# Optimization experiments

Hardware: AMD Instinct MI355X
Metric: run time of the kernel (lower is better)

The kernel has to match this reference:

```python
import jax, jax.numpy as jnp
import numpy as np

N = 80000
E = 1280000
C_IN, HID, C_OUT = 3, 64, 1
DEPTH = 3
KS = [40000, 20000, 10000]  # ceil(0.5 * n) per pooling level
EPS = 1e-5


def gcn_conv(x, W, src, dst, ew, n, fill=2.0):
    # PyG GCNConv with add_self_loops=True; improved => self-loop weight fill=2.0
    h = x @ W                                           # [n, F]
    deg = jax.ops.segment_sum(ew, dst, num_segments=n) + fill
    dinv = jax.lax.rsqrt(deg)
    norm = dinv[src] * ew * dinv[dst]                   # [E]
    agg = jax.ops.segment_sum(norm[:, None] * h[src], dst, num_segments=n)
    return agg + (fill * dinv * dinv)[:, None] * h      # self-loop term


def batchnorm(x, gamma, beta):
    # BatchNorm1d in training mode: biased batch stats over the node dim
    mu = jnp.mean(x, axis=0)
    var = jnp.var(x, axis=0)
    return gamma * (x - mu) * jax.lax.rsqrt(var + EPS) + beta


def gcn_block(x, src, dst, ew, n, W, gamma, beta, fill=2.0):
    return jax.nn.relu(batchnorm(gcn_conv(x, W, src, dst, ew, n, fill), gamma, beta))


def topk_pool(x, src, dst, ew, w, k):
    # TopKPooling with ReLU nonlinearity: score = relu(x.w / ||w||)
    n = x.shape[0]
    score = jax.nn.relu(x @ w / jnp.linalg.norm(w))
    sc, perm = jax.lax.top_k(score, k)
    xk = x[perm] * sc[:, None]
    # filter_adj with fixed edge count: invalid edges get weight 0 (no-op in GCN)
    mapping = jnp.full((n,), -1, dtype=src.dtype).at[perm].set(
        jnp.arange(k, dtype=src.dtype))
    ns, nd = mapping[src], mapping[dst]
    valid = (ns >= 0) & (nd >= 0)
    ns = jnp.where(valid, ns, 0)
    nd = jnp.where(valid, nd, 0)
    new_ew = jnp.where(valid, ew, jnp.zeros((), ew.dtype))
    return xk, ns, nd, new_ew, perm


def _forward(x, edge_index, Wd, gd, bd, pw, Wu, gu, bu, W_out):
    src, dst = edge_index[0], edge_index[1]
    ew = jnp.ones(src.shape, x.dtype)
    n = x.shape[0]
    x = gcn_block(x, src, dst, ew, n, Wd[0], gd[0], bd[0])
    xs, sds, ews, perms = [x], [(src, dst)], [ew], []
    for i in range(DEPTH):
        x, src, dst, ew, perm = topk_pool(x, src, dst, ew, pw[i], KS[i])
        x = gcn_block(x, src, dst, ew, KS[i], Wd[i + 1], gd[i + 1], bd[i + 1])
        if i < DEPTH - 1:
            xs.append(x); sds.append((src, dst)); ews.append(ew)
        perms.append(perm)
    for i in range(DEPTH):
        j = DEPTH - 1 - i
        res = xs[j]; src, dst = sds[j]; ew = ews[j]; perm = perms[j]
        up = jnp.zeros_like(res).at[perm].set(x)
        x = res + up
        if i < DEPTH - 1:
            x = gcn_block(x, src, dst, ew, res.shape[0], Wu[i], gu[i], bu[i])
        else:
            x = jax.nn.sigmoid(
                gcn_conv(x, W_out, src, dst, ew, res.shape[0], fill=1.0))
    return x


def setup_inputs() -> dict:
    key = jax.random.key(0)
    ks = jax.random.split(key, 16)
    nrm = lambda k, shape: jax.random.normal(k, shape, jnp.float32) * 0.1
    inp = {
        "x": jax.random.normal(ks[0], (N, C_IN), jnp.float32),
        "edge_index": jax.random.randint(ks[1], (2, E), 0, N, jnp.int32),
    }
    dims = [(C_IN, HID)] + [(HID, HID)] * DEPTH
    ki = 2
    for l, (a, b) in enumerate(dims):
        inp[f"W_d{l}"] = nrm(ks[ki], (a, b)); ki += 1
        inp[f"g_d{l}"] = jnp.ones((b,), jnp.float32)
        inp[f"b_d{l}"] = jnp.zeros((b,), jnp.float32)
    for l in range(DEPTH):
        inp[f"pw{l}"] = nrm(ks[ki], (HID,)); ki += 1
    for l in range(DEPTH - 1):
        inp[f"W_u{l}"] = nrm(ks[ki], (HID, HID)); ki += 1
        inp[f"g_u{l}"] = jnp.ones((HID,), jnp.float32)
        inp[f"b_u{l}"] = jnp.zeros((HID,), jnp.float32)
    inp["W_out"] = nrm(ks[ki], (HID, C_OUT))
    return inp


def reference(x, edge_index, W_d0, g_d0, b_d0, W_d1, g_d1, b_d1, W_d2, g_d2,
              b_d2, W_d3, g_d3, b_d3, pw0, pw1, pw2, W_u0, g_u0, b_u0,
              W_u1, g_u1, b_u1, W_out):
    Wd = [W_d0, W_d1, W_d2, W_d3]
    gd = [g_d0, g_d1, g_d2, g_d3]
    bd = [b_d0, b_d1, b_d2, b_d3]
    pw = [pw0, pw1, pw2]
    Wu = [W_u0, W_u1]
    gu = [g_u0, g_u1]
    bu = [b_u0, b_u1]
    return _forward(x, edge_index, Wd, gd, bd, pw, Wu, gu, bu, W_out)
```

## Files before the change

### kernel.cpp

```cpp
#include <hip/hip_runtime.h>
#include <cstdint>

#define NN0 80000
#define NE 1280000
#define MMB_GRID 2048
#define EB 2048
#define ENB 625

static inline int cdiv(int a, int b){ return (a+b-1)/b; }

__global__ void k_ehist6(const int* __restrict__ key, int* __restrict__ hist, int shift){
  __shared__ int lh[64];
  if (threadIdx.x < 64) lh[threadIdx.x] = 0;
  __syncthreads();
  int base = blockIdx.x*EB + threadIdx.x;
  #pragma unroll
  for (int u = 0; u < 8; u++)
    atomicAdd(&lh[(key[base + u*256] >> shift) & 63], 1);
  __syncthreads();
  if (threadIdx.x < 64) hist[threadIdx.x*ENB + blockIdx.x] = lh[threadIdx.x];
}

__global__ void k_scan_part(const int* __restrict__ in, int* __restrict__ bsum, int n){
  __shared__ int ws[256];
  int base = blockIdx.x*2048 + threadIdx.x*8;
  int s = 0;
  #pragma unroll
  for (int u = 0; u < 8; u++){ int i = base+u; if (i < n) s += in[i]; }
  ws[threadIdx.x] = s; __syncthreads();
  for (int st = 128; st > 0; st >>= 1){
    if (threadIdx.x < st) ws[threadIdx.x] += ws[threadIdx.x+st];
    __syncthreads();
  }
  if (threadIdx.x == 0) bsum[blockIdx.x] = ws[0];
}

__global__ void k_scan_fin_flat(int* __restrict__ data, const int* __restrict__ bsum, int nb, int n){
  __shared__ int bws[256]; __shared__ int ws[256];
  int t = threadIdx.x;
  bws[t] = (t < nb) ? bsum[t] : 0; __syncthreads();
  for (int st = 1; st < 256; st <<= 1){
    int a = (t >= st) ? bws[t-st] : 0; __syncthreads();
    bws[t] += a; __syncthreads();
  }
  int blockoff = (blockIdx.x == 0) ? 0 : bws[blockIdx.x-1];
  int base = blockIdx.x*2048 + t*8;
  int v[8]; int s = 0;
  #pragma unroll
  for (int u = 0; u < 8; u++){ int i = base+u; v[u] = (i < n) ? data[i] : 0; s += v[u]; }
  ws[t] = s; __syncthreads();
  for (int st = 1; st < 256; st <<= 1){
    int a = (t >= st) ? ws[t-st] : 0; __syncthreads();
    ws[t] += a; __syncthreads();
  }
  int off = blockoff + ws[t] - s;
  #pragma unroll
  for (int u = 0; u < 8; u++){
    int i = base+u;
    if (i < n){ data[i] = off; off += v[u]; }
  }
}

__global__ void k_escatter6(const int* __restrict__ keyin, const int* __restrict__ valin,
                            int* __restrict__ keyout, int* __restrict__ valout,
                            const int* __restrict__ hist, int shift){
  __shared__ int dbase[64], run[64], wcnt[4][64];
  int t = threadIdx.x, lane = t & 63, w = t >> 6;
  if (t < 64){ dbase[t] = hist[t*ENB + blockIdx.x]; run[t] = 0; }
  __syncthreads();
  for (int u = 0; u < 8; u++){
    if (t < 64){ wcnt[0][t]=0; wcnt[1][t]=0; wcnt[2][t]=0; wcnt[3][t]=0; }
    __syncthreads();
    int g = blockIdx.x*EB + u*256 + t;
    int kk = keyin[g], vv = valin[g];
    int d = (kk >> shift) & 63;
    unsigned long long m = ~0ull;
    #pragma unroll
    for (int b = 0; b < 6; b++){
      unsigned long long bal = __ballot((d >> b) & 1);
      m &= ((d >> b) & 1) ? bal : ~bal;
    }
    int rnk = __popcll(m & ((1ull << lane) - 1ull));
    if (rnk == 0) wcnt[w][d] = __popcll(m);
    __syncthreads();
    int off2 = run[d] + rnk;
    for (int w2 = 0; w2 < w; w2++) off2 += wcnt[w2][d];
    int pos = dbase[d] + off2;
    keyout[pos] = kk; valout[pos] = vv;
    __syncthreads();
    if (t < 64) run[t] += wcnt[0][t] + wcnt[1][t] + wcnt[2][t] + wcnt[3][t];
    __syncthreads();
  }
}

__global__ __launch_bounds__(1024) void k_bucket_build(
    const int* __restrict__ ek, const int* __restrict__ ev,
    const int* __restrict__ hist_s,
    int* __restrict__ rp, int* __restrict__ col,
    float* __restrict__ dA, float* __restrict__ dB, int n){
  __shared__ int cnt[2048];
  __shared__ int sa[1024], sb[1024];
  int b = blockIdx.x, t = threadIdx.x;
  int gb = hist_s[b*ENB];
  int ge = hist_s[(b+1)*ENB];
  int n0 = b*2048;
  cnt[t] = 0; cnt[t+1024] = 0;
  __syncthreads();
  for (int e = gb + t; e < ge; e += 1024)
    atomicAdd(&cnt[ek[e] - n0], 1);
  __syncthreads();
  int v0 = cnt[2*t], v1 = cnt[2*t+1];
  int s = v0 + v1;
  sa[t] = s; __syncthreads();
  int* cu = sa; int* ot = sb;
  for (int st = 1; st < 1024; st <<= 1){
    ot[t] = cu[t] + ((t >= st) ? cu[t-st] : 0);
    __syncthreads();
    int* tmp = cu; cu = ot; ot = tmp;
  }
  int base2 = cu[t] - s;
  int p0 = base2, p1 = base2 + v0;
  int nn = n - n0; if (nn > 2048) nn = 2048;
  cnt[2*t]   = gb + p0;
  cnt[2*t+1] = gb + p1;
  int i0 = n0 + 2*t;
  if (2*t < nn){
    rp[i0] = gb + p0;
    dA[i0] = 1.0f/sqrtf((float)v0 + 2.f);
    dB[i0] = 1.0f/sqrtf((float)v0 + 1.f);
  }
  if (2*t+1 < nn){
    rp[i0+1] = gb + p1;
    dA[i0+1] = 1.0f/sqrtf((float)v1 + 2.f);
    dB[i0+1] = 1.0f/sqrtf((float)v1 + 1.f);
  }
  if (b == (int)gridDim.x - 1 && t == 0) rp[n] = ge;
  __syncthreads();
  for (int e = gb + t; e < ge; e += 1024){
    int d = ek[e];
    int pos = atomicAdd(&cnt[d - n0], 1);
    col[pos] = ev[e];
  }
}

__global__ void k_scan_rp(const int* __restrict__ in, int* __restrict__ rp,
                          int* __restrict__ cur, float* __restrict__ dA,
                          float* __restrict__ dB, int n){
  __shared__ int ws[256];
  int t = threadIdx.x;
  int pre = blockIdx.x*2048;
  int s = 0;
  for (int i = t; i < pre; i += 256) s += in[i];
  ws[t] = s; __syncthreads();
  for (int st = 128; st > 0; st >>= 1){
    if (t < st) ws[t] += ws[t+st];
    __syncthreads();
  }
  int blockoff = ws[0];
  __syncthreads();
  int base = pre + t*8;
  int v[8]; int ls = 0;
  #pragma unroll
  for (int u = 0; u < 8; u++){ int i = base+u; v[u] = (i < n) ? in[i] : 0; ls += v[u]; }
  ws[t] = ls; __syncthreads();
  for (int st = 1; st < 256; st <<= 1){
    int a = (t >= st) ? ws[t-st] : 0; __syncthreads();
    ws[t] += a; __syncthreads();
  }
  int off = blockoff + ws[t] - ls;
  #pragma unroll
  for (int u = 0; u < 8; u++){
    int i = base+u;
    if (i < n){
      rp[i] = off;
      if (cur) cur[i] = off;
      off += v[u];
      dA[i] = 1.0f/sqrtf((float)v[u] + 2.f);
      if (dB) dB[i] = 1.0f/sqrtf((float)v[u] + 1.f);
      if (i == n-1) rp[n] = off;
    }
  }
}

__global__ void k_conv64(const int* __restrict__ rp, const int* __restrict__ col,
                         const float* __restrict__ dinv, const float* __restrict__ x,
                         const float* __restrict__ W, float* __restrict__ out,
                         float* __restrict__ part, int n){
  __shared__ float yl[4][64];
  __shared__ float ls[64], lq[64];
  int lane = threadIdx.x & 63, w = threadIdx.x >> 6;
  if (threadIdx.x < 64){ ls[threadIdx.x] = 0.f; lq[threadIdx.x] = 0.f; }
  __syncthreads();
  float sa = 0.f, sq = 0.f;
  int wid = blockIdx.x*4 + w, nw = gridDim.x*4;
  for (int i = wid; i < n; i += nw){
    int beg = rp[i], end = rp[i+1];
    float di = dinv[i];
    float y = 0.f;
    int j = beg;
    for (; j + 4 <= end; j += 4){
      int s0 = col[j], s1 = col[j+1], s2 = col[j+2], s3 = col[j+3];
      float y0 = dinv[s0]*x[s0*64+lane];
      float y1 = dinv[s1]*x[s1*64+lane];
      float y2 = dinv[s2]*x[s2*64+lane];
      float y3 = dinv[s3]*x[s3*64+lane];
      y += (y0+y1) + (y2+y3);
    }
    for (; j < end; j++){ int s = col[j]; y += dinv[s]*x[s*64+lane]; }
    y = di*y + 2.f*di*di*x[i*64+lane];
    yl[w][lane] = y;
    float acc = 0.f;
    #pragma unroll
    for (int k2 = 0; k2 < 64; k2++)
      acc += yl[w][k2]*W[k2*64+lane];
    out[i*64+lane] = acc;
    sa += acc; sq += acc*acc;
  }
  atomicAdd(&ls[lane], sa); atomicAdd(&lq[lane], sq);
  __syncthreads();
  if (threadIdx.x < 128)
    part[blockIdx.x*128 + threadIdx.x] =
      (threadIdx.x < 64) ? ls[threadIdx.x] : lq[threadIdx.x-64];
}

__global__ void k_conv3(const int* __restrict__ rp, const int* __restrict__ col,
                        const float* __restrict__ dinv, const float* __restrict__ x,
                        const float* __restrict__ W, float* __restrict__ out,
                        float* __restrict__ part, int n){
  __shared__ float ls[64], lq[64];
  int lane = threadIdx.x & 63, w = threadIdx.x >> 6;
  if (threadIdx.x < 64){ ls[threadIdx.x] = 0.f; lq[threadIdx.x] = 0.f; }
  __syncthreads();
  float wf0 = W[lane], wf1 = W[64+lane], wf2 = W[128+lane];
  float sa = 0.f, sq = 0.f;
  int wid = blockIdx.x*4 + w, nw = gridDim.x*4;
  for (int i = wid; i < n; i += nw){
    int beg = rp[i], end = rp[i+1];
    float a0 = 0.f, a1 = 0.f, a2 = 0.f;
    for (int j = beg + lane; j < end; j += 64){
      int s2 = col[j];
      float ds = dinv[s2];
      a0 += ds*x[s2*3+0]; a1 += ds*x[s2*3+1]; a2 += ds*x[s2*3+2];
    }
    for (int o = 32; o > 0; o >>= 1){
      a0 += __shfl_xor(a0, o); a1 += __shfl_xor(a1, o); a2 += __shfl_xor(a2, o);
    }
    float di = dinv[i];
    float sl = 2.f*di*di;
    a0 = di*a0 + sl*x[i*3+0];
    a1 = di*a1 + sl*x[i*3+1];
    a2 = di*a2 + sl*x[i*3+2];
    float s = a0*wf0 + a1*wf1 + a2*wf2;
    out[i*64+lane] = s; sa += s; sq += s*s;
  }
  atomicAdd(&ls[lane], sa); atomicAdd(&lq[lane], sq);
  __syncthreads();
  if (threadIdx.x < 128)
    part[blockIdx.x*128 + threadIdx.x] =
      (threadIdx.x < 64) ? ls[threadIdx.x] : lq[threadIdx.x-64];
}

__global__ void k_stats_reduce(const float* __restrict__ part, float* __restrict__ stats){
  int c = blockIdx.x, lane = threadIdx.x;
  float s = 0.f;
  for (int b = lane; b < MMB_GRID; b += 64) s += part[b*128 + c];
  for (int o = 32; o > 0; o >>= 1) s += __shfl_xor(s, o);
  if (lane == 0) stats[c] = s;
}

__global__ void k_bnrelu_score(float* __restrict__ x, const float* __restrict__ stats,
                               const float* __restrict__ gamma, const float* __restrict__ beta,
                               const float* __restrict__ pw,
                               float* __restrict__ score, unsigned* __restrict__ key,
                               int* __restrict__ idx, int n, int P){
  int lane = threadIdx.x & 63, w = threadIdx.x >> 6;
  int wid = blockIdx.x*4 + w, nw = gridDim.x*4;
  float inv_n = 1.f/(float)n;
  float mu = stats[lane]*inv_n;
  float var = stats[64+lane]*inv_n - mu*mu;
  float gs = gamma[lane]*(1.f/sqrtf(var+1e-5f));
  float bt = beta[lane];
  float pv = pw[lane];
  float q = pv*pv;
  for (int o = 32; o > 0; o >>= 1) q += __shfl_xor(q, o);
  float qn = 1.f/sqrtf(q);
  for (int i = wid; i < n; i += nw){
    float v = fmaxf(gs*(x[i*64+lane]-mu)+bt, 0.f);
    x[i*64+lane] = v;
    float s = v*pv;
    for (int o = 32; o > 0; o >>= 1) s += __shfl_xor(s, o);
    if (lane == 0){
      float sc = fmaxf(s*qn, 0.f);
      score[i] = sc; key[i] = ~__float_as_uint(sc); idx[i] = i;
    }
  }
  for (int g = n + wid; g < P; g += nw)
    if (lane == 0){ key[g] = 0xFFFFFFFFu; idx[g] = 0; }
}

__global__ void k_radix_hist(const unsigned* __restrict__ key, int* __restrict__ hist,
                             int shift, int nblk){
  __shared__ int lh[256];
  lh[threadIdx.x] = 0; __syncthreads();
  int base = blockIdx.x*1024 + threadIdx.x;
  #pragma unroll
  for (int u = 0; u < 4; u++){
    unsigned d = (key[base + u*256] >> shift) & 255u;
    atomicAdd(&lh[d], 1);
  }
  __syncthreads();
  hist[threadIdx.x*nblk + blockIdx.x] = lh[threadIdx.x];
}

__global__ void k_radix_scatter(const unsigned* __restrict__ keyin, const int* __restrict__ idxin,
                                unsigned* __restrict__ keyout, int* __restrict__ idxout,
                                const int* __restrict__ hist, int shift, int nblk){
  __shared__ int dbase[256], run[256], sc[256];
  __shared__ int wcnt[4][256];
  int t = threadIdx.x, lane = t & 63, w = t >> 6;
  int pre = 0, tot = 0;
  for (int b = 0; b < nblk; b++){
    int v = hist[t*nblk + b];
    if (b < blockIdx.x) pre += v;
    tot += v;
  }
  sc[t] = tot; __syncthreads();
  for (int st = 1; st < 256; st <<= 1){
    int a = (t >= st) ? sc[t-st] : 0; __syncthreads();
    sc[t] += a; __syncthreads();
  }
  dbase[t] = sc[t] - tot + pre;
  run[t] = 0;
  for (int u = 0; u < 4; u++){
    wcnt[0][t] = 0; wcnt[1][t] = 0; wcnt[2][t] = 0; wcnt[3][t] = 0;
    __syncthreads();
    int g = blockIdx.x*1024 + u*256 + t;
    unsigned kk = keyin[g]; int id = idxin[g];
    unsigned d = (kk >> shift) & 255u;
    unsigned long long m = ~0ull;
    #pragma unroll
    for (int b = 0; b < 8; b++){
      unsigned long long bal = __ballot((d >> b) & 1u);
      m &= ((d >> b) & 1u) ? bal : ~bal;
    }
    int rnk = __popcll(m & ((1ull << lane) - 1ull));
    if (rnk == 0) wcnt[w][d] = __popcll(m);
    __syncthreads();
    int off2 = run[d] + rnk;
    for (int w2 = 0; w2 < w; w2++) off2 += wcnt[w2][d];
    int pos = dbase[d] + off2;
    keyout[pos] = kk; idxout[pos] = id;
    __syncthreads();
    run[t] += wcnt[0][t] + wcnt[1][t] + wcnt[2][t] + wcnt[3][t];
    __syncthreads();
  }
}

__global__ void k_select_gather(const int* __restrict__ idxs, const float* __restrict__ x,
                                const float* __restrict__ score, int* __restrict__ perm,
                                int* __restrict__ mapv, float* __restrict__ xk, int n, int k){
  int t = blockIdx.x*blockDim.x + threadIdx.x;
  if (t < n){
    int i = idxs[t];
    mapv[i] = (t < k) ? t : -1;
    if (t < k) perm[t] = i;
  }
  if (t < k*64){
    int r = t >> 6, f = t & 63;
    int i = idxs[r];
    xk[t] = x[i*64+f]*score[i];
  }
}

__global__ void k_hist_mapped(const int* __restrict__ rp_p, const int* __restrict__ col_p,
                              const int* __restrict__ mapv, int* __restrict__ indeg, int np){
  int d = blockIdx.x*blockDim.x + threadIdx.x;
  if (d >= np) return;
  int md = mapv[d];
  if (md < 0) return;
  int c = 0, e = rp_p[d+1];
  int j = rp_p[d];
  for (; j + 4 <= e; j += 4){
    int c0 = (mapv[col_p[j]]   >= 0);
    int c1 = (mapv[col_p[j+1]] >= 0);
    int c2 = (mapv[col_p[j+2]] >= 0);
    int c3 = (mapv[col_p[j+3]] >= 0);
    c += (c0+c1) + (c2+c3);
  }
  for (; j < e; j++) if (mapv[col_p[j]] >= 0) c++;
  indeg[md] = c;
}

__global__ void k_scatter_mapped(const int* __restrict__ rp_p, const int* __restrict__ col_p,
                                 const int* __restrict__ mapv, const int* __restrict__ rp_c,
                                 int* __restrict__ col_c, int np){
  int d = blockIdx.x*blockDim.x + threadIdx.x;
  if (d >= np) return;
  int md = mapv[d];
  if (md < 0) return;
  int pos = rp_c[md], e = rp_p[d+1];
  int j = rp_p[d];
  for (; j + 4 <= e; j += 4){
    int m0 = mapv[col_p[j]], m1 = mapv[col_p[j+1]];
    int m2 = mapv[col_p[j+2]], m3 = mapv[col_p[j+3]];
    if (m0 >= 0) col_c[pos++] = m0;
    if (m1 >= 0) col_c[pos++] = m1;
    if (m2 >= 0) col_c[pos++] = m2;
    if (m3 >= 0) col_c[pos++] = m3;
  }
  for (; j < e; j++){
    int ms = mapv[col_p[j]];
    if (ms >= 0) col_c[pos++] = ms;
  }
}

__global__ void k_bnrelu_scatter(const float* __restrict__ x, const float* __restrict__ stats,
                                 const float* __restrict__ gamma, const float* __restrict__ beta,
                                 const int* __restrict__ perm, float* __restrict__ res, int n){
  int t = blockIdx.x*blockDim.x + threadIdx.x;
  if (t >= n*64) return;
  int r = t >> 6, f = t & 63;
  float inv_n = 1.0f/(float)n;
  float mu = stats[f]*inv_n;
  float var = stats[64+f]*inv_n - mu*mu;
  float v = gamma[f]*(x[t]-mu)*(1.0f/sqrtf(var+1e-5f)) + beta[f];
  res[perm[r]*64+f] += fmaxf(v, 0.f);
}

__global__ void k_matvec(const float* __restrict__ x, const float* __restrict__ W,
                         float* __restrict__ h1, int n){
  int lane = threadIdx.x & 63, w = threadIdx.x >> 6;
  int wid = blockIdx.x*4 + w, nw = gridDim.x*4;
  float wv = W[lane];
  for (int i = wid; i < n; i += nw){
    float v = x[i*64+lane]*wv;
    for (int o = 32; o > 0; o >>= 1) v += __shfl_xor(v, o);
    if (lane == 0) h1[i] = v;
  }
}

__global__ void k_gather_sig(const int* __restrict__ rp, const int* __restrict__ col,
                             const float* __restrict__ dinv, const float* __restrict__ h1,
                             float* __restrict__ out, int n){
  int i = blockIdx.x*blockDim.x + threadIdx.x;
  if (i >= n) return;
  int beg = rp[i], end = rp[i+1];
  float di = dinv[i];
  float acc = 0.f;
  int j = beg;
  for (; j + 4 <= end; j += 4){
    int s0 = col[j], s1 = col[j+1], s2 = col[j+2], s3 = col[j+3];
    float v0 = dinv[s0]*h1[s0];
    float v1 = dinv[s1]*h1[s1];
    float v2 = dinv[s2]*h1[s2];
    float v3 = dinv[s3]*h1[s3];
    acc += (v0+v1) + (v2+v3);
  }
  for (; j < end; j++) acc += dinv[col[j]]*h1[col[j]];
  float v = di*acc + di*di*h1[i];
  out[i] = 1.f/(1.f+expf(-v));
}


extern "C" void kernel_launch(void* const* d_in, const int* in_sizes, int n_in,
                              void* d_out, int out_size, void* d_ws, size_t ws_size,
                              hipStream_t stream) {
  const float* x_in = (const float*)d_in[0];
  const int* ei = (const int*)d_in[1];
  const int* src0 = ei;
  const int* dst0 = ei + NE;
  const float* W_d[4] = {(const float*)d_in[2],(const float*)d_in[5],(const float*)d_in[8],(const float*)d_in[11]};
  const float* g_d[4] = {(const float*)d_in[3],(const float*)d_in[6],(const float*)d_in[9],(const float*)d_in[12]};
  const float* b_d[4] = {(const float*)d_in[4],(const float*)d_in[7],(const float*)d_in[10],(const float*)d_in[13]};
  const float* pw[3]  = {(const float*)d_in[14],(const float*)d_in[15],(const float*)d_in[16]};
  const float* W_u[2] = {(const float*)d_in[17],(const float*)d_in[20]};
  const float* g_u[2] = {(const float*)d_in[18],(const float*)d_in[21]};
  const float* b_u[2] = {(const float*)d_in[19],(const float*)d_in[22]};
  const float* W_out  = (const float*)d_in[23];
  float* out = (float*)d_out;

  float* base = (float*)d_ws;
  size_t off = 0;
  auto alloc = [&](size_t nf){ float* p = base + off; off += nf; return p; };
  float* x0 = alloc(5120000);
  float* x1 = alloc(2560000);
  float* x2 = alloc(1280000);
  float* x3 = alloc(640000);
  float* A  = alloc(2560000);
  int* col0 = (int*)alloc(NE);
  int* col1 = (int*)alloc(NE);
  int* col2 = (int*)alloc(NE);
  int* col3 = (int*)alloc(NE);
  int* ek1 = (int*)alloc(NE);
  int* ev1 = (int*)alloc(NE);
  int* rp0 = (int*)alloc(80001);
  int* rp1 = (int*)alloc(40001);
  int* rp2 = (int*)alloc(20001);
  int* rp3 = (int*)alloc(10001);
  int* indeg  = (int*)alloc(NN0);
  float* dinv0  = alloc(NN0);
  float* dinv0f = alloc(NN0);
  float* dinv1  = alloc(40000);
  float* dinv2  = alloc(20000);
  float* dinv3  = alloc(10000);
  float* score = alloc(NN0);
  int* mapv = (int*)alloc(NN0);
  int* p0 = (int*)alloc(40000);
  int* p1 = (int*)alloc(20000);
  int* p2 = (int*)alloc(10000);
  float* stats = alloc(128);
  float* part  = alloc(MMB_GRID*128);
  unsigned* keyA = (unsigned*)alloc(81920);
  unsigned* keyB = (unsigned*)alloc(81920);
  int* idxA = (int*)alloc(81920);
  int* idxB = (int*)alloc(81920);
  int* hist = (int*)alloc(81920);
  int* ehist = (int*)alloc(64*ENB);
  int* bsum = (int*)alloc(256);
  (void)ws_size; (void)in_sizes; (void)n_in; (void)out_size;

  const int B = 256;

  k_ehist6<<<ENB, B, 0, stream>>>(dst0, ehist, 11);
  {
    int nb = cdiv(64*ENB, 2048);
    k_scan_part    <<<nb, B, 0, stream>>>(ehist, bsum, 64*ENB);
    k_scan_fin_flat<<<nb, B, 0, stream>>>(ehist, bsum, nb, 64*ENB);
  }
  k_escatter6<<<ENB, B, 0, stream>>>(dst0, src0, ek1, ev1, ehist, 11);
  k_bucket_build<<<cdiv(NN0,2048), 1024, 0, stream>>>(ek1, ev1, ehist, rp0, col0,
                                                      dinv0, dinv0f, NN0);

  auto conv = [&](const float* xin, const float* W, int n,
                  const int* rp, const int* col, const float* dv, float* dstb){
    k_conv64<<<MMB_GRID, B, 0, stream>>>(rp, col, dv, xin, W, dstb, part, n);
    k_stats_reduce<<<128, 64, 0, stream>>>(part, stats);
  };

  auto pool = [&](float* xb, const float* gm, const float* bt, const float* pwv,
                  int n, int k, int* pm){
    int nblk = cdiv(n, 1024), P = nblk*1024;
    k_bnrelu_score<<<1024, B, 0, stream>>>(xb, stats, gm, bt, pwv, score, keyA, idxA, n, P);
    unsigned* ka = keyA; int* ia = idxA; unsigned* kb = keyB; int* ib = idxB;
    for (int pass = 0; pass < 4; pass++){
      k_radix_hist   <<<nblk, B, 0, stream>>>(ka, hist, pass*8, nblk);
      k_radix_scatter<<<nblk, B, 0, stream>>>(ka, ia, kb, ib, hist, pass*8, nblk);
      unsigned* tk = ka; ka = kb; kb = tk;
      int* ti = ia; ia = ib; ib = ti;
    }
    k_select_gather<<<cdiv(k*64,B), B, 0, stream>>>(ia, xb, score, pm, mapv, A, n, k);
  };

  auto csr_mapped = [&](const int* rp_p, const int* col_p, int np, int nc,
                        int* rp_c, int* col_c, float* dv){
    k_hist_mapped<<<cdiv(np,B), B, 0, stream>>>(rp_p, col_p, mapv, indeg, np);
    k_scan_rp<<<cdiv(nc,2048), B, 0, stream>>>(indeg, rp_c, nullptr, dv, nullptr, nc);
    k_scatter_mapped<<<cdiv(np,B), B, 0, stream>>>(rp_p, col_p, mapv, rp_c, col_c, np);
  };

  k_conv3<<<MMB_GRID, B, 0, stream>>>(rp0, col0, dinv0, x_in, W_d[0], x0, part, NN0);
  k_stats_reduce<<<128, 64, 0, stream>>>(part, stats);
  pool(x0, g_d[0], b_d[0], pw[0], NN0, 40000, p0);
  csr_mapped(rp0, col0, NN0, 40000, rp1, col1, dinv1);

  conv(A, W_d[1], 40000, rp1, col1, dinv1, x1);
  pool(x1, g_d[1], b_d[1], pw[1], 40000, 20000, p1);
  csr_mapped(rp1, col1, 40000, 20000, rp2, col2, dinv2);

  conv(A, W_d[2], 20000, rp2, col2, dinv2, x2);
  pool(x2, g_d[2], b_d[2], pw[2], 20000, 10000, p2);
  csr_mapped(rp2, col2, 20000, 10000, rp3, col3, dinv3);

  conv(A, W_d[3], 10000, rp3, col3, dinv3, x3);

  k_bnrelu_scatter<<<cdiv(10000*64,B), B, 0, stream>>>(x3, stats, g_d[3], b_d[3], p2, x2, 10000);
  conv(x2, W_u[0], 20000, rp2, col2, dinv2, A);
  k_bnrelu_scatter<<<cdiv(20000*64,B), B, 0, stream>>>(A, stats, g_u[0], b_u[0], p1, x1, 20000);
  conv(x1, W_u[1], 40000, rp1, col1, dinv1, A);
  k_bnrelu_scatter<<<cdiv(40000*64,B), B, 0, stream>>>(A, stats, g_u[1], b_u[1], p0, x0, 40000);

  float* h1 = score;
  k_matvec<<<512, B, 0, stream>>>(x0, W_out, h1, NN0);
  k_gather_sig<<<cdiv(NN0,B), B, 0, stream>>>(rp0, col0, dinv0f, h1, out, NN0);
}
```

Baseline: 743.2 us.

## Use 11-bit radix top-k with fused histogram/gather and global-atomic CSR build

Replaces the 4-pass 8-bit radix sort for top-k with three 11-bit passes. The first histogram is fused into the BN/ReLU/score kernel, and the final scatter directly writes perm, mapping and the scaled gathered features, dropping the separate select/gather kernel. The level-0 CSR build now counts in-degrees with global atomics during the edge bucketing, then scans and scatters with global atomic cursors instead of the shared-memory bucket builder. Conv grid sizes also now scale with the graph level. The changes cut kernel launches and passes, but add larger shared histograms, 11-iteration ballot ranking, and global atomic contention on the edge scatter.

```diff
diff --git a/kernel.cpp b/kernel.cpp
--- a/kernel.cpp
+++ b/kernel.cpp
@@ -3,13 +3,17 @@
 
 #define NN0 80000
 #define NE 1280000
-#define MMB_GRID 2048
 #define EB 2048
 #define ENB 625
+#define RD 2048
+#define RDM 2047
 
 static inline int cdiv(int a, int b){ return (a+b-1)/b; }
 
-__global__ void k_ehist6(const int* __restrict__ key, int* __restrict__ hist, int shift){
+__global__ void k_ehist6(const int* __restrict__ key, int* __restrict__ hist, int shift,
+                         int* __restrict__ indeg){
+  for (int i = blockIdx.x*blockDim.x + threadIdx.x; i < NN0; i += gridDim.x*blockDim.x)
+    indeg[i] = 0;
   __shared__ int lh[64];
   if (threadIdx.x < 64) lh[threadIdx.x] = 0;
   __syncthreads();
@@ -63,7 +67,8 @@
 
 __global__ void k_escatter6(const int* __restrict__ keyin, const int* __restrict__ valin,
                             int* __restrict__ keyout, int* __restrict__ valout,
-                            const int* __restrict__ hist, int shift){
+                            const int* __restrict__ hist, int shift,
+                            int* __restrict__ indeg){
   __shared__ int dbase[64], run[64], wcnt[4][64];
   int t = threadIdx.x, lane = t & 63, w = t >> 6;
   if (t < 64){ dbase[t] = hist[t*ENB + blockIdx.x]; run[t] = 0; }
@@ -87,58 +92,18 @@
     for (int w2 = 0; w2 < w; w2++) off2 += wcnt[w2][d];
     int pos = dbase[d] + off2;
     keyout[pos] = kk; valout[pos] = vv;
+    atomicAdd(&indeg[kk], 1);
     __syncthreads();
     if (t < 64) run[t] += wcnt[0][t] + wcnt[1][t] + wcnt[2][t] + wcnt[3][t];
     __syncthreads();
   }
 }
 
-__global__ __launch_bounds__(1024) void k_bucket_build(
-    const int* __restrict__ ek, const int* __restrict__ ev,
-    const int* __restrict__ hist_s,
-    int* __restrict__ rp, int* __restrict__ col,
-    float* __restrict__ dA, float* __restrict__ dB, int n){
-  __shared__ int cnt[2048];
-  __shared__ int sa[1024], sb[1024];
-  int b = blockIdx.x, t = threadIdx.x;
-  int gb = hist_s[b*ENB];
-  int ge = hist_s[(b+1)*ENB];
-  int n0 = b*2048;
-  cnt[t] = 0; cnt[t+1024] = 0;
-  __syncthreads();
-  for (int e = gb + t; e < ge; e += 1024)
-    atomicAdd(&cnt[ek[e] - n0], 1);
-  __syncthreads();
-  int v0 = cnt[2*t], v1 = cnt[2*t+1];
-  int s = v0 + v1;
-  sa[t] = s; __syncthreads();
-  int* cu = sa; int* ot = sb;
-  for (int st = 1; st < 1024; st <<= 1){
-    ot[t] = cu[t] + ((t >= st) ? cu[t-st] : 0);
-    __syncthreads();
-    int* tmp = cu; cu = ot; ot = tmp;
-  }
-  int base2 = cu[t] - s;
-  int p0 = base2, p1 = base2 + v0;
-  int nn = n - n0; if (nn > 2048) nn = 2048;
-  cnt[2*t]   = gb + p0;
-  cnt[2*t+1] = gb + p1;
-  int i0 = n0 + 2*t;
-  if (2*t < nn){
-    rp[i0] = gb + p0;
-    dA[i0] = 1.0f/sqrtf((float)v0 + 2.f);
-    dB[i0] = 1.0f/sqrtf((float)v0 + 1.f);
-  }
-  if (2*t+1 < nn){
-    rp[i0+1] = gb + p1;
-    dA[i0+1] = 1.0f/sqrtf((float)v1 + 2.f);
-    dB[i0+1] = 1.0f/sqrtf((float)v1 + 1.f);
-  }
-  if (b == (int)gridDim.x - 1 && t == 0) rp[n] = ge;
-  __syncthreads();
-  for (int e = gb + t; e < ge; e += 1024){
+__global__ void k_escat_local(const int* __restrict__ ek, const int* __restrict__ ev,
+                              int* __restrict__ cur, int* __restrict__ col){
+  for (int e = blockIdx.x*blockDim.x + threadIdx.x; e < NE; e += gridDim.x*blockDim.x){
     int d = ek[e];
-    int pos = atomicAdd(&cnt[d - n0], 1);
+    int pos = atomicAdd(&cur[d], 1);
     col[pos] = ev[e];
   }
 }
@@ -260,10 +225,10 @@
       (threadIdx.x < 64) ? ls[threadIdx.x] : lq[threadIdx.x-64];
 }
 
-__global__ void k_stats_reduce(const float* __restrict__ part, float* __restrict__ stats){
+__global__ void k_stats_reduce(const float* __restrict__ part, float* __restrict__ stats, int nb){
   int c = blockIdx.x, lane = threadIdx.x;
   float s = 0.f;
-  for (int b = lane; b < MMB_GRID; b += 64) s += part[b*128 + c];
+  for (int b = lane; b < nb; b += 64) s += part[b*128 + c];
   for (int o = 32; o > 0; o >>= 1) s += __shfl_xor(s, o);
   if (lane == 0) stats[c] = s;
 }
@@ -272,9 +237,12 @@
                                const float* __restrict__ gamma, const float* __restrict__ beta,
                                const float* __restrict__ pw,
                                float* __restrict__ score, unsigned* __restrict__ key,
-                               int* __restrict__ idx, int n, int P){
-  int lane = threadIdx.x & 63, w = threadIdx.x >> 6;
-  int wid = blockIdx.x*4 + w, nw = gridDim.x*4;
+                               int* __restrict__ idx, int* __restrict__ hist,
+                               int n, int nblk){
+  __shared__ int lh[RD];
+  int t = threadIdx.x, lane = t & 63, w = t >> 6;
+  #pragma unroll
+  for (int j = 0; j < 8; j++) lh[t*8+j] = 0;
   float inv_n = 1.f/(float)n;
   float mu = stats[lane]*inv_n;
   float var = stats[64+lane]*inv_n - mu*mu;
@@ -284,64 +252,106 @@
   float q = pv*pv;
   for (int o = 32; o > 0; o >>= 1) q += __shfl_xor(q, o);
   float qn = 1.f/sqrtf(q);
-  for (int i = wid; i < n; i += nw){
-    float v = fmaxf(gs*(x[i*64+lane]-mu)+bt, 0.f);
-    x[i*64+lane] = v;
-    float s = v*pv;
-    for (int o = 32; o > 0; o >>= 1) s += __shfl_xor(s, o);
-    if (lane == 0){
-      float sc = fmaxf(s*qn, 0.f);
-      score[i] = sc; key[i] = ~__float_as_uint(sc); idx[i] = i;
-    }
-  }
-  for (int g = n + wid; g < P; g += nw)
-    if (lane == 0){ key[g] = 0xFFFFFFFFu; idx[g] = 0; }
-}
-
-__global__ void k_radix_hist(const unsigned* __restrict__ key, int* __restrict__ hist,
-                             int shift, int nblk){
-  __shared__ int lh[256];
-  lh[threadIdx.x] = 0; __syncthreads();
-  int base = blockIdx.x*1024 + threadIdx.x;
-  #pragma unroll
+  __syncthreads();
+  int P = nblk*1024;
+  int base = blockIdx.x*1024 + w*256;
+  for (int t2 = 0; t2 < 256; t2++){
+    int i = base + t2;
+    if (i < n){
+      float v = fmaxf(gs*(x[i*64+lane]-mu)+bt, 0.f);
+      x[i*64+lane] = v;
+      float s = v*pv;
+      for (int o = 32; o > 0; o >>= 1) s += __shfl_xor(s, o);
+      if (lane == 0){
+        float sc = fmaxf(s*qn, 0.f);
+        unsigned kk = ~__float_as_uint(sc);
+        score[i] = sc; key[i] = kk; idx[i] = i;
+        atomicAdd(&lh[kk & RDM], 1);
+      }
+    } else if (i < P){
+      if (lane == 0){
+        key[i] = 0xFFFFFFFFu; idx[i] = 0;
+        atomicAdd(&lh[RDM], 1);
+      }
+    }
+  }
+  __syncthreads();
+  #pragma unroll
+  for (int j = 0; j < 8; j++)
+    hist[(t*8+j)*nblk + blockIdx.x] = lh[t*8+j];
+}
+
+__global__ void k_radix_hist11(const unsigned* __restrict__ key, int* __restrict__ hist,
+                               int shift, int nblk){
+  __shared__ int lh[RD];
+  int t = threadIdx.x;
+  #pragma unroll
+  for (int j = 0; j < 8; j++) lh[t*8+j] = 0;
+  __syncthreads();
+  int base = blockIdx.x*1024 + t;
+  #pragma unroll
+  for (int u = 0; u < 4; u++)
+    atomicAdd(&lh[(key[base + u*256] >> shift) & RDM], 1);
+  __syncthreads();
+  #pragma unroll
+  for (int j = 0; j < 8; j++)
+    hist[(t*8+j)*nblk + blockIdx.x] = lh[t*8+j];
+}
+
+__global__ void k_radix_scatter11(const unsigned* __restrict__ keyin, const int* __restrict__ idxin,
+                                  unsigned* __restrict__ keyout, int* __restrict__ idxout,
+                                  const int* __restrict__ hist, int shift, int nblk,
+                                  int fin, const float* __restrict__ x,
+                                  const float* __restrict__ score,
+                                  int* __restrict__ perm, int* __restrict__ mapv,
+                                  float* __restrict__ xk, int n, int k){
+  __shared__ int dbase[RD], run[RD], wcnt[4][RD];
+  __shared__ int ssum[256], stmp[256];
+  int t = threadIdx.x, lane = t & 63, w = t >> 6;
+  int b = blockIdx.x;
+  int pre[8], tot[8];
+  #pragma unroll
+  for (int j = 0; j < 8; j++){ pre[j] = 0; tot[j] = 0; }
+  for (int blk = 0; blk < nblk; blk++){
+    #pragma unroll
+    for (int j = 0; j < 8; j++){
+      int v = hist[(t*8+j)*nblk + blk];
+      tot[j] += v;
+      if (blk < b) pre[j] += v;
+    }
+  }
+  int S = 0; int ex[8];
+  #pragma unroll
+  for (int j = 0; j < 8; j++){ ex[j] = S; S += tot[j]; }
+  ssum[t] = S; __syncthreads();
+  int* cu = ssum; int* ot = stmp;
+  for (int st = 1; st < 256; st <<= 1){
+    ot[t] = cu[t] + ((t >= st) ? cu[t-st] : 0);
+    __syncthreads();
+    int* tmp = cu; cu = ot; ot = tmp;
+  }
+  int exS = cu[t] - S;
+  #pragma unroll
+  for (int j = 0; j < 8; j++){
+    dbase[t*8+j] = exS + ex[j] + pre[j];
+    run[t*8+j] = 0;
+  }
+  __syncthreads();
   for (int u = 0; u < 4; u++){
-    unsigned d = (key[base + u*256] >> shift) & 255u;
-    atomicAdd(&lh[d], 1);
-  }
-  __syncthreads();
-  hist[threadIdx.x*nblk + blockIdx.x] = lh[threadIdx.x];
-}
-
-__global__ void k_radix_scatter(const unsigned* __restrict__ keyin, const int* __restrict__ idxin,
-                                unsigned* __restrict__ keyout, int* __restrict__ idxout,
-                                const int* __restrict__ hist, int shift, int nblk){
-  __shared__ int dbase[256], run[256], sc[256];
-  __shared__ int wcnt[4][256];
-  int t = threadIdx.x, lane = t & 63, w = t >> 6;
-  int pre = 0, tot = 0;
-  for (int b = 0; b < nblk; b++){
-    int v = hist[t*nblk + b];
-    if (b < blockIdx.x) pre += v;
-    tot += v;
-  }
-  sc[t] = tot; __syncthreads();
-  for (int st = 1; st < 256; st <<= 1){
-    int a = (t >= st) ? sc[t-st] : 0; __syncthreads();
-    sc[t] += a; __syncthreads();
-  }
-  dbase[t] = sc[t] - tot + pre;
-  run[t] = 0;
-  for (int u = 0; u < 4; u++){
-    wcnt[0][t] = 0; wcnt[1][t] = 0; wcnt[2][t] = 0; wcnt[3][t] = 0;
-    __syncthreads();
-    int g = blockIdx.x*1024 + u*256 + t;
+    #pragma unroll
+    for (int j = 0; j < 8; j++){
+      int bb = t*8+j;
+      wcnt[0][bb] = 0; wcnt[1][bb] = 0; wcnt[2][bb] = 0; wcnt[3][bb] = 0;
+    }
+    __syncthreads();
+    int g = b*1024 + u*256 + t;
     unsigned kk = keyin[g]; int id = idxin[g];
-    unsigned d = (kk >> shift) & 255u;
+    int d = (kk >> shift) & RDM;
     unsigned long long m = ~0ull;
     #pragma unroll
-    for (int b = 0; b < 8; b++){
-      unsigned long long bal = __ballot((d >> b) & 1u);
-      m &= ((d >> b) & 1u) ? bal : ~bal;
+    for (int bit = 0; bit < 11; bit++){
+      unsigned long long bal = __ballot((d >> bit) & 1);
+      m &= ((d >> bit) & 1) ? bal : ~bal;
     }
     int rnk = __popcll(m & ((1ull << lane) - 1ull));
     if (rnk == 0) wcnt[w][d] = __popcll(m);
@@ -349,26 +359,30 @@
     int off2 = run[d] + rnk;
     for (int w2 = 0; w2 < w; w2++) off2 += wcnt[w2][d];
     int pos = dbase[d] + off2;
-    keyout[pos] = kk; idxout[pos] = id;
-    __syncthreads();
-    run[t] += wcnt[0][t] + wcnt[1][t] + wcnt[2][t] + wcnt[3][t];
-    __syncthreads();
-  }
-}
-
-__global__ void k_select_gather(const int* __restrict__ idxs, const float* __restrict__ x,
-                                const float* __restrict__ score, int* __restrict__ perm,
-                                int* __restrict__ mapv, float* __restrict__ xk, int n, int k){
-  int t = blockIdx.x*blockDim.x + threadIdx.x;
-  if (t < n){
-    int i = idxs[t];
-    mapv[i] = (t < k) ? t : -1;
-    if (t < k) perm[t] = i;
-  }
-  if (t < k*64){
-    int r = t >> 6, f = t & 63;
-    int i = idxs[r];
-    xk[t] = x[i*64+f]*score[i];
+    if (!fin){
+      keyout[pos] = kk; idxout[pos] = id;
+    } else if (pos < n){
+      mapv[id] = (pos < k) ? pos : -1;
+      if (pos < k){
+        perm[pos] = id;
+        float sc = score[id];
+        const float4* xr = (const float4*)(x + (size_t)id*64);
+        float4* xo = (float4*)(xk + (size_t)pos*64);
+        #pragma unroll
+        for (int f = 0; f < 16; f++){
+          float4 vv = xr[f];
+          vv.x *= sc; vv.y *= sc; vv.z *= sc; vv.w *= sc;
+          xo[f] = vv;
+        }
+      }
+    }
+    __syncthreads();
+    #pragma unroll
+    for (int j = 0; j < 8; j++){
+      int bb = t*8+j;
+      run[bb] += wcnt[0][bb] + wcnt[1][bb] + wcnt[2][bb] + wcnt[3][bb];
+    }
+    __syncthreads();
   }
 }
 
@@ -497,6 +511,7 @@
   int* rp1 = (int*)alloc(40001);
   int* rp2 = (int*)alloc(20001);
   int* rp3 = (int*)alloc(10001);
+  int* cur0 = (int*)alloc(NN0);
   int* indeg  = (int*)alloc(NN0);
   float* dinv0  = alloc(NN0);
   float* dinv0f = alloc(NN0);
@@ -509,46 +524,47 @@
   int* p1 = (int*)alloc(20000);
   int* p2 = (int*)alloc(10000);
   float* stats = alloc(128);
-  float* part  = alloc(MMB_GRID*128);
+  float* part  = alloc(2048*128);
   unsigned* keyA = (unsigned*)alloc(81920);
   unsigned* keyB = (unsigned*)alloc(81920);
   int* idxA = (int*)alloc(81920);
   int* idxB = (int*)alloc(81920);
-  int* hist = (int*)alloc(81920);
+  int* hist = (int*)alloc(RD*80);
   int* ehist = (int*)alloc(64*ENB);
   int* bsum = (int*)alloc(256);
   (void)ws_size; (void)in_sizes; (void)n_in; (void)out_size;
 
   const int B = 256;
 
-  k_ehist6<<<ENB, B, 0, stream>>>(dst0, ehist, 11);
+  k_ehist6<<<ENB, B, 0, stream>>>(dst0, ehist, 11, indeg);
   {
     int nb = cdiv(64*ENB, 2048);
     k_scan_part    <<<nb, B, 0, stream>>>(ehist, bsum, 64*ENB);
     k_scan_fin_flat<<<nb, B, 0, stream>>>(ehist, bsum, nb, 64*ENB);
   }
-  k_escatter6<<<ENB, B, 0, stream>>>(dst0, src0, ek1, ev1, ehist, 11);
-  k_bucket_build<<<cdiv(NN0,2048), 1024, 0, stream>>>(ek1, ev1, ehist, rp0, col0,
-                                                      dinv0, dinv0f, NN0);
-
-  auto conv = [&](const float* xin, const float* W, int n,
+  k_escatter6<<<ENB, B, 0, stream>>>(dst0, src0, ek1, ev1, ehist, 11, indeg);
+  k_scan_rp<<<cdiv(NN0,2048), B, 0, stream>>>(indeg, rp0, cur0, dinv0, dinv0f, NN0);
+  k_escat_local<<<1024, B, 0, stream>>>(ek1, ev1, cur0, col0);
+
+  auto conv = [&](const float* xin, const float* W, int n, int nb,
                   const int* rp, const int* col, const float* dv, float* dstb){
-    k_conv64<<<MMB_GRID, B, 0, stream>>>(rp, col, dv, xin, W, dstb, part, n);
-    k_stats_reduce<<<128, 64, 0, stream>>>(part, stats);
+    k_conv64<<<nb, B, 0, stream>>>(rp, col, dv, xin, W, dstb, part, n);
+    k_stats_reduce<<<128, 64, 0, stream>>>(part, stats, nb);
   };
 
   auto pool = [&](float* xb, const float* gm, const float* bt, const float* pwv,
                   int n, int k, int* pm){
-    int nblk = cdiv(n, 1024), P = nblk*1024;
-    k_bnrelu_score<<<1024, B, 0, stream>>>(xb, stats, gm, bt, pwv, score, keyA, idxA, n, P);
-    unsigned* ka = keyA; int* ia = idxA; unsigned* kb = keyB; int* ib = idxB;
-    for (int pass = 0; pass < 4; pass++){
-      k_radix_hist   <<<nblk, B, 0, stream>>>(ka, hist, pass*8, nblk);
-      k_radix_scatter<<<nblk, B, 0, stream>>>(ka, ia, kb, ib, hist, pass*8, nblk);
-      unsigned* tk = ka; ka = kb; kb = tk;
-      int* ti = ia; ia = ib; ib = ti;
-    }
-    k_select_gather<<<cdiv(k*64,B), B, 0, stream>>>(ia, xb, score, pm, mapv, A, n, k);
+    int nblk = cdiv(n, 1024);
+    k_bnrelu_score<<<nblk, B, 0, stream>>>(xb, stats, gm, bt, pwv, score, keyA, idxA,
+                                           hist, n, nblk);
+    k_radix_scatter11<<<nblk, B, 0, stream>>>(keyA, idxA, keyB, idxB, hist, 0, nblk,
+                                              0, nullptr, nullptr, nullptr, nullptr, nullptr, n, k);
+    k_radix_hist11<<<nblk, B, 0, stream>>>(keyB, hist, 11, nblk);
+    k_radix_scatter11<<<nblk, B, 0, stream>>>(keyB, idxB, keyA, idxA, hist, 11, nblk,
+                                              0, nullptr, nullptr, nullptr, nullptr, nullptr, n, k);
+    k_radix_hist11<<<nblk, B, 0, stream>>>(keyA, hist, 22, nblk);
+    k_radix_scatter11<<<nblk, B, 0, stream>>>(keyA, idxA, keyB, idxB, hist, 22, nblk,
+                                              1, xb, score, pm, mapv, A, n, k);
   };
 
   auto csr_mapped = [&](const int* rp_p, const int* col_p, int np, int nc,
@@ -558,25 +574,25 @@
     k_scatter_mapped<<<cdiv(np,B), B, 0, stream>>>(rp_p, col_p, mapv, rp_c, col_c, np);
   };
 
-  k_conv3<<<MMB_GRID, B, 0, stream>>>(rp0, col0, dinv0, x_in, W_d[0], x0, part, NN0);
-  k_stats_reduce<<<128, 64, 0, stream>>>(part, stats);
+  k_conv3<<<2048, B, 0, stream>>>(rp0, col0, dinv0, x_in, W_d[0], x0, part, NN0);
+  k_stats_reduce<<<128, 64, 0, stream>>>(part, stats, 2048);
   pool(x0, g_d[0], b_d[0], pw[0], NN0, 40000, p0);
   csr_mapped(rp0, col0, NN0, 40000, rp1, col1, dinv1);
 
-  conv(A, W_d[1], 40000, rp1, col1, dinv1, x1);
+  conv(A, W_d[1], 40000, 2048, rp1, col1, dinv1, x1);
   pool(x1, g_d[1], b_d[1], pw[1], 40000, 20000, p1);
   csr_mapped(rp1, col1, 40000, 20000, rp2, col2, dinv2);
 
-  conv(A, W_d[2], 20000, rp2, col2, dinv2, x2);
+  conv(A, W_d[2], 20000, 1024, rp2, col2, dinv2, x2);
   pool(x2, g_d[2], b_d[2], pw[2], 20000, 10000, p2);
   csr_mapped(rp2, col2, 20000, 10000, rp3, col3, dinv3);
 
-  conv(A, W_d[3], 10000, rp3, col3, dinv3, x3);
+  conv(A, W_d[3], 10000, 512, rp3, col3, dinv3, x3);
 
   k_bnrelu_scatter<<<cdiv(10000*64,B), B, 0, stream>>>(x3, stats, g_d[3], b_d[3], p2, x2, 10000);
-  conv(x2, W_u[0], 20000, rp2, col2, dinv2, A);
+  conv(x2, W_u[0], 20000, 1024, rp2, col2, dinv2, A);
   k_bnrelu_scatter<<<cdiv(20000*64,B), B, 0, stream>>>(A, stats, g_u[0], b_u[0], p1, x1, 20000);
-  conv(x1, W_u[1], 40000, rp1, col1, dinv1, A);
+  conv(x1, W_u[1], 40000, 2048, rp1, col1, dinv1, A);
   k_bnrelu_scatter<<<cdiv(40000*64,B), B, 0, stream>>>(A, stats, g_u[1], b_u[1], p0, x0, 40000);
 
   float* h1 = score;
```

Result: slower. 1.631 ms (+119.5%).
